# Performance work log

Hardware: AMD Instinct MI355X
Metric: run time of the kernel (lower is better)

## Reference

```python
import jax, jax.numpy as jnp
import numpy as np

# --- Mamba2Enc config (matches init_kwargs + mamba_ssm Mamba2 defaults) ---
D_IN = 1024
D_MODEL = 512
N_CLASSES = 2
NLAYERS = 2
D_STATE = 64
D_CONV = 4
EXPAND = 2
HEADDIM = 64
D_INNER = EXPAND * D_MODEL            # 1024
NHEADS = D_INNER // HEADDIM           # 16
CONV_DIM = D_INNER + 2 * D_STATE      # 1152 (ngroups=1)
D_IN_PROJ = 2 * D_INNER + 2 * D_STATE + NHEADS  # 2192
EPS = 1e-5


def setup_inputs() -> dict:
    key = jax.random.key(0)
    ks = jax.random.split(key, 10)
    def w(k, shape, sc=0.02):
        return jax.random.normal(k, shape, jnp.float32) * sc
    x = jax.random.normal(ks[0], (4, 4096, D_IN), jnp.float32)
    # fc1
    W1 = w(ks[1], (D_MODEL, D_IN))
    b1 = jnp.zeros((D_MODEL,), jnp.float32)
    # per-layer params stacked on leading NLAYERS axis
    ln_w = jnp.ones((NLAYERS, D_MODEL), jnp.float32)
    ln_b = jnp.zeros((NLAYERS, D_MODEL), jnp.float32)
    W_in = w(ks[2], (NLAYERS, D_IN_PROJ, D_MODEL))
    conv_w = w(ks[3], (NLAYERS, CONV_DIM, D_CONV), 0.1)
    conv_b = jnp.zeros((NLAYERS, CONV_DIM), jnp.float32)
    # dt_bias so that softplus(dt_bias) ~ [0.001, 0.1] (mamba init range)
    dt_bias = jax.random.uniform(ks[4], (NLAYERS, NHEADS), jnp.float32, -6.0, -2.3)
    A_log = jnp.log(jnp.tile(jnp.arange(1, NHEADS + 1, dtype=jnp.float32), (NLAYERS, 1)))
    Dskip = jnp.ones((NLAYERS, NHEADS), jnp.float32)
    norm_w = jnp.ones((NLAYERS, D_INNER), jnp.float32)
    W_out = w(ks[5], (NLAYERS, D_MODEL, D_INNER))
    # classifier
    Wc = w(ks[6], (N_CLASSES, D_MODEL))
    bc = jnp.zeros((N_CLASSES,), jnp.float32)
    return dict(x=x, W1=W1, b1=b1, ln_w=ln_w, ln_b=ln_b, W_in=W_in,
                conv_w=conv_w, conv_b=conv_b, dt_bias=dt_bias, A_log=A_log,
                Dskip=Dskip, norm_w=norm_w, W_out=W_out, Wc=Wc, bc=bc)


def _layernorm(h, w, b):
    mu = jnp.mean(h, axis=-1, keepdims=True)
    var = jnp.mean(jnp.square(h - mu), axis=-1, keepdims=True)
    return (h - mu) * jax.lax.rsqrt(var + EPS) * w + b


def _silu(x):
    return x * jax.nn.sigmoid(x)


def _mamba2(x, W_in, conv_w, conv_b, dt_bias, A_log, Dskip, norm_w, W_out):
    b, l, _ = x.shape
    zxbcdt = jnp.einsum('bld,ed->ble', x, W_in)  # (b, l, D_IN_PROJ)
    z = zxbcdt[..., :D_INNER]
    xBC = zxbcdt[..., D_INNER:D_INNER + CONV_DIM]
    dt = jax.nn.softplus(zxbcdt[..., -NHEADS:] + dt_bias)  # (b, l, h)
    # causal depthwise conv1d (kernel D_CONV) + silu
    xp = jnp.pad(xBC, ((0, 0), (D_CONV - 1, 0), (0, 0)))
    xBC = sum(xp[:, k:k + l, :] * conv_w[:, k] for k in range(D_CONV)) + conv_b
    xBC = _silu(xBC)
    xh = xBC[..., :D_INNER].reshape(b, l, NHEADS, HEADDIM)
    B = xBC[..., D_INNER:D_INNER + D_STATE]   # (b, l, n) ngroups=1
    C = xBC[..., D_INNER + D_STATE:]          # (b, l, n)
    A = -jnp.exp(A_log)                       # (h,)
    dA = jnp.exp(dt * A)                      # (b, l, h)
    dtx = dt[..., None] * xh                  # (b, l, h, p)

    def step(hstate, inp):
        dA_t, dtx_t, B_t, C_t = inp  # (b,h), (b,h,p), (b,n), (b,n)
        hstate = hstate * dA_t[:, :, None, None] + dtx_t[:, :, None, :] * B_t[:, None, :, None]
        y = jnp.einsum('bn,bhnp->bhp', C_t, hstate)
        return hstate, y

    init = jnp.zeros((b, NHEADS, D_STATE, HEADDIM), x.dtype)
    xs = (dA.transpose(1, 0, 2), dtx.transpose(1, 0, 2, 3),
          B.transpose(1, 0, 2), C.transpose(1, 0, 2))
    _, ys = jax.lax.scan(step, init, xs)      # ys: (l, b, h, p)
    y = ys.transpose(1, 0, 2, 3) + Dskip[None, None, :, None] * xh
    y = y.reshape(b, l, D_INNER)
    # RMSNormGated (norm_before_gate=False): rmsnorm(y * silu(z)) * weight
    y = y * _silu(z)
    y = y * jax.lax.rsqrt(jnp.mean(jnp.square(y), axis=-1, keepdims=True) + EPS) * norm_w
    return jnp.einsum('ble,de->bld', y, W_out)


def reference(x, W1, b1, ln_w, ln_b, W_in, conv_w, conv_b, dt_bias, A_log,
              Dskip, norm_w, W_out, Wc, bc):
    # fc1: Linear + GELU (dropout is identity at eval)
    h = jax.nn.gelu(jnp.einsum('bli,di->bld', x, W1) + b1, approximate=False)
    for i in range(NLAYERS):
        h = h + _mamba2(_layernorm(h, ln_w[i], ln_b[i]), W_in[i], conv_w[i],
                        conv_b[i], dt_bias[i], A_log[i], Dskip[i], norm_w[i], W_out[i])
    return jnp.einsum('bld,cd->blc', h, Wc) + bc
```

## Files before the change

kernel.cpp:

```cpp
#include <hip/hip_runtime.h>
#include <hip/hip_bf16.h>
#include <math.h>

#define BATCH 4
#define SEQ 4096
#define ROWS 16384
#define DIN 1024
#define DMODEL 512
#define DINNER 1024
#define DSTATE 64
#define NH 16
#define HD 64
#define CONVDIM 1152
#define DPROJ 2192
#define NPAD 2304
#define QC 64
#define NCH 64
#define LD 72

typedef __attribute__((ext_vector_type(8))) __bf16 bf16x8;
typedef __attribute__((ext_vector_type(4))) __bf16 bf16x4;
typedef __attribute__((ext_vector_type(4))) float f32x4;

__device__ __forceinline__ float siluf(float x){ return x / (1.f + __expf(-x)); }
__device__ __forceinline__ float geluf(float x){ return 0.5f*x*(1.f + erff(x*0.70710678118654752440f)); }

__device__ __forceinline__ bf16x8 scale8(bf16x8 v, float s){
  bf16x8 r;
  #pragma unroll
  for (int e = 0; e < 8; e++) r[e] = (__bf16)((float)v[e]*s);
  return r;
}

__device__ __forceinline__ void gl_lds16(const void* g, void* l){
  __builtin_amdgcn_global_load_lds((const __attribute__((address_space(1))) void*)g,
                                   (__attribute__((address_space(3))) void*)l, 16, 0, 0);
}

__global__ void cast_bf16_kernel(const float* __restrict__ src, __bf16* __restrict__ dst, long n){
  long i = (long)blockIdx.x*blockDim.x + threadIdx.x;
  long stride = (long)gridDim.x*blockDim.x;
  for (; i < n; i += stride) dst[i] = (__bf16)src[i];
}

__global__ void pad_win_kernel(const float* __restrict__ src, __bf16* __restrict__ dst){
  long total = 2L*NPAD*DMODEL;
  long i = (long)blockIdx.x*blockDim.x + threadIdx.x;
  long stride = (long)gridDim.x*blockDim.x;
  for (; i < total; i += stride){
    int k = (int)(i % DMODEL);
    int n = (int)((i / DMODEL) % NPAD);
    int l = (int)(i / ((long)DMODEL*NPAD));
    float v = (n < DPROJ) ? src[((long)l*DPROJ + n)*DMODEL + k] : 0.f;
    dst[i] = (__bf16)v;
  }
}

template<typename OutT, int EPI, int BM, int BN>
__global__ __launch_bounds__(256) void gemm_bt(const __bf16* __restrict__ A, const __bf16* __restrict__ Bm,
                                               OutT* __restrict__ C, const float* __restrict__ bias,
                                               int K, int Nc){
  constexpr int MI = BM/32, NI = BN/32;
  constexpr int CHA = BM/64;
  constexpr int CHT = (BM+BN)/64;
  __shared__ __align__(16) __bf16 As[BM*32];
  __shared__ __align__(16) __bf16 Bs[BN*32];
  int bm = blockIdx.x, bn = blockIdx.y;
  int tid = threadIdx.x;
  int lane = tid & 63, wid = tid >> 6;
  int wm = (wid >> 1)*(BM/2), wn = (wid & 1)*(BN/2);
  int lr = lane & 15, kb = lane >> 4;
  f32x4 acc[MI][NI] = {};
  const char* Ab = (const char*)A + (size_t)bm*BM*(size_t)(K*2);
  const char* Bb = (const char*)Bm + (size_t)bn*BN*(size_t)(K*2);
  int nkk = K >> 5;
  for (int kk = 0; kk < nkk; kk++){
    #pragma unroll
    for (int it = 0; it < CHT; it++){
      int cbase = it*4096 + wid*1024;
      int off = cbase + lane*16;
      int row = off >> 6, cb = off & 63;
      if (it < CHA) gl_lds16(Ab + (size_t)row*(K*2) + kk*64 + cb, (char*)As + cbase);
      else          gl_lds16(Bb + (size_t)(row - BM)*(K*2) + kk*64 + cb, (char*)Bs + (cbase - BM*64));
    }
    __syncthreads();
    bf16x8 af[MI], bfr[NI];
    #pragma unroll
    for (int mi = 0; mi < MI; mi++) af[mi] = *(const bf16x8*)(As + (wm + mi*16 + lr)*32 + kb*8);
    #pragma unroll
    for (int ni = 0; ni < NI; ni++) bfr[ni] = *(const bf16x8*)(Bs + (wn + ni*16 + lr)*32 + kb*8);
    #pragma unroll
    for (int mi = 0; mi < MI; mi++)
      #pragma unroll
      for (int ni = 0; ni < NI; ni++)
        acc[mi][ni] = __builtin_amdgcn_mfma_f32_16x16x32_bf16(af[mi], bfr[ni], acc[mi][ni], 0, 0, 0);
    __syncthreads();
  }
  #pragma unroll
  for (int mi = 0; mi < MI; mi++){
    #pragma unroll
    for (int ni = 0; ni < NI; ni++){
      int r0 = bm*BM + wm + mi*16 + (lane >> 4)*4;
      int c  = bn*BN + wn + ni*16 + lr;
      if (c < Nc){
        OutT* Cp = C + (size_t)r0*Nc + c;
        #pragma unroll
        for (int j = 0; j < 4; j++){
          float v = acc[mi][ni][j];
          if (EPI == 1){ float u = v + bias[c]; v = geluf(u); }
          if (EPI == 2){ v += (float)Cp[(size_t)j*Nc]; }
          Cp[(size_t)j*Nc] = (OutT)v;
        }
      }
    }
  }
}

__global__ __launch_bounds__(256) void ln_kernel(const float* __restrict__ h, const float* __restrict__ w,
                                                 const float* __restrict__ b, __bf16* __restrict__ out){
  int row = blockIdx.x*4 + (threadIdx.x >> 6);
  int lane = threadIdx.x & 63;
  const float* hr = h + (size_t)row*DMODEL + lane*8;
  float4 a = *(const float4*)hr, a2 = *(const float4*)(hr+4);
  float v[8] = {a.x,a.y,a.z,a.w,a2.x,a2.y,a2.z,a2.w};
  float s = 0.f;
  #pragma unroll
  for (int i = 0; i < 8; i++) s += v[i];
  #pragma unroll
  for (int o = 32; o; o >>= 1) s += __shfl_xor(s, o, 64);
  float mu = s*(1.f/512.f);
  float q = 0.f;
  #pragma unroll
  for (int i = 0; i < 8; i++){ float d = v[i]-mu; q += d*d; }
  #pragma unroll
  for (int o = 32; o; o >>= 1) q += __shfl_xor(q, o, 64);
  float rs = rsqrtf(q*(1.f/512.f) + 1e-5f);
  const float* wp = w + lane*8; const float* bp = b + lane*8;
  bf16x8 o8;
  #pragma unroll
  for (int i = 0; i < 8; i++) o8[i] = (__bf16)((v[i]-mu)*rs*wp[i] + bp[i]);
  *(bf16x8*)(out + (size_t)row*DMODEL + lane*8) = o8;
}

__global__ __launch_bounds__(256) void conv_bc(const __bf16* __restrict__ zx, const float* __restrict__ cw,
                                               const float* __restrict__ cb, __bf16* __restrict__ BCc){
  int idx = blockIdx.x*256 + threadIdx.x;
  int j = idx & 127;
  long bt = idx >> 7;
  int t = (int)(bt & (SEQ-1));
  int ch = DINNER + j;
  const __bf16* src = zx + (size_t)bt*DPROJ + 2048 + j;
  float acc = cb[ch] + (float)src[0]*cw[ch*4+3];
  if (t >= 1) acc += (float)src[-1L*DPROJ]*cw[ch*4+2];
  if (t >= 2) acc += (float)src[-2L*DPROJ]*cw[ch*4+1];
  if (t >= 3) acc += (float)src[-3L*DPROJ]*cw[ch*4+0];
  BCc[idx] = (__bf16)siluf(acc);
}

__global__ __launch_bounds__(256) void dt_kernel(const __bf16* __restrict__ zx, const float* __restrict__ dt_bias,
                                                 float* __restrict__ dtT){
  int idx = blockIdx.x*256 + threadIdx.x;
  int hh = idx & (NH-1); long bt = idx >> 4;
  int b = (int)(bt >> 12); int t = (int)(bt & (SEQ-1));
  float v = (float)zx[(size_t)bt*DPROJ + (DPROJ-NH) + hh] + dt_bias[hh];
  float sp = (v > 20.f) ? v : log1pf(__expf(v));
  dtT[((size_t)b*NH + hh)*SEQ + t] = sp;
}

__global__ __launch_bounds__(128) void ssd_state(const __bf16* __restrict__ zx, const __bf16* __restrict__ BCc,
                                                 const float* __restrict__ dtT, const float* __restrict__ A_log,
                                                 const float* __restrict__ cw, const float* __restrict__ cb,
                                                 __bf16* __restrict__ Schunk, float* __restrict__ Pbuf,
                                                 __bf16* __restrict__ xhT){
  __shared__ __align__(16) __bf16 Bt_all[2][64*LD];
  __shared__ __align__(16) __bf16 Xt_all[2][64*LD];
  int widx = threadIdx.x >> 6, lane = threadIdx.x & 63;
  int c = blockIdx.x*2 + widx, h = blockIdx.y, b = blockIdx.z;
  __bf16* Bt = Bt_all[widx];
  __bf16* Xt = Xt_all[widx];
  int lr = lane & 15, kb = lane >> 4, hi4 = lane >> 4;
  long t0 = (long)c*QC;
  size_t bt0 = (size_t)b*SEQ + t0;
  int bh = b*NH + h;
  float Ac = -expf(A_log[h]);
  float dtv = dtT[(size_t)bh*SEQ + t0 + lane];
  float cum = dtv*Ac;
  #pragma unroll
  for (int off = 1; off < 64; off <<= 1){ float v = __shfl_up(cum, off, 64); if (lane >= off) cum += v; }
  float cumQ = __shfl(cum, 63, 64);
  float w = __expf(cumQ - cum) * dtv;
  {
    const __bf16* bp = BCc + bt0*128 + lane;
    for (int tb = 0; tb < 8; tb++){
      bf16x8 buf;
      #pragma unroll
      for (int u = 0; u < 8; u++){
        int t = tb*8 + u;
        float bv = (float)bp[(size_t)t*128];
        buf[u] = (__bf16)(bv * __shfl(w, t, 64));
      }
      *(bf16x8*)&Bt[lane*LD + tb*8] = buf;
    }
  }
  {
    int ch = h*HD + lane;
    float w0 = cw[ch*4], w1 = cw[ch*4+1], w2 = cw[ch*4+2], w3 = cw[ch*4+3], cbv = cb[ch];
    const __bf16* xp = zx + bt0*DPROJ + (DINNER + ch);
    float x1 = (t0 >= 1) ? (float)xp[-1L*DPROJ] : 0.f;
    float x2 = (t0 >= 2) ? (float)xp[-2L*DPROJ] : 0.f;
    float x3 = (t0 >= 3) ? (float)xp[-3L*DPROJ] : 0.f;
    __bf16* xo = xhT + ((size_t)bh*NCH + c)*4096 + lane*64;
    for (int tb = 0; tb < 8; tb++){
      bf16x8 buf;
      #pragma unroll
      for (int u = 0; u < 8; u++){
        int t = tb*8 + u;
        float x0 = (float)xp[(size_t)t*DPROJ];
        float xv = siluf(cbv + w3*x0 + w2*x1 + w1*x2 + w0*x3);
        x3 = x2; x2 = x1; x1 = x0;
        buf[u] = (__bf16)xv;
      }
      *(bf16x8*)&Xt[lane*LD + tb*8] = buf;
      *(bf16x8*)(xo + tb*8) = buf;
    }
  }
  f32x4 acc[4][4] = {};
  #pragma unroll
  for (int kk = 0; kk < 2; kk++){
    bf16x8 af[4], bfr[4];
    #pragma unroll
    for (int mi = 0; mi < 4; mi++) af[mi]  = *(bf16x8*)&Bt[(mi*16+lr)*LD + kk*32 + kb*8];
    #pragma unroll
    for (int ni = 0; ni < 4; ni++) bfr[ni] = *(bf16x8*)&Xt[(ni*16+lr)*LD + kk*32 + kb*8];
    #pragma unroll
    for (int mi = 0; mi < 4; mi++)
      #pragma unroll
      for (int ni = 0; ni < 4; ni++)
        acc[mi][ni] = __builtin_amdgcn_mfma_f32_16x16x32_bf16(af[mi], bfr[ni], acc[mi][ni], 0, 0, 0);
  }
  __bf16* Sp = Schunk + ((size_t)bh*NCH + c)*4096;
  #pragma unroll
  for (int mi = 0; mi < 4; mi++)
    #pragma unroll
    for (int ni = 0; ni < 4; ni++){
      int n0 = mi*16 + hi4*4;
      int p  = ni*16 + lr;
      bf16x4 v;
      #pragma unroll
      for (int r = 0; r < 4; r++) v[r] = (__bf16)acc[mi][ni][r];
      *(bf16x4*)&Sp[p*64 + n0] = v;
    }
  if (lane == 0) Pbuf[bh*NCH + c] = __expf(cumQ);
}

__global__ __launch_bounds__(64) void ssd_comb(__bf16* __restrict__ Schunk, const float* __restrict__ Pbuf){
  int bh = blockIdx.x >> 4;
  int eb = blockIdx.x & 15;
  int e = eb*256 + threadIdx.x*4;
  __bf16* base = Schunk + (size_t)bh*NCH*4096 + e;
  float T0 = 0.f, T1 = 0.f, T2 = 0.f, T3 = 0.f;
  for (int c = 0; c < NCH; c++){
    float P = Pbuf[bh*NCH + c];
    bf16x4* p = (bf16x4*)(base + (size_t)c*4096);
    bf16x4 s = *p;
    bf16x4 o; o[0] = (__bf16)T0; o[1] = (__bf16)T1; o[2] = (__bf16)T2; o[3] = (__bf16)T3;
    *p = o;
    T0 = T0*P + (float)s[0]; T1 = T1*P + (float)s[1];
    T2 = T2*P + (float)s[2]; T3 = T3*P + (float)s[3];
  }
}

__global__ __launch_bounds__(256) void ssd_y(const __bf16* __restrict__ BCc, const float* __restrict__ dtT,
                                             const float* __restrict__ A_log, const float* __restrict__ Dskip,
                                             const __bf16* __restrict__ xhT, const __bf16* __restrict__ Spre,
                                             __bf16* __restrict__ yout){
  __shared__ __align__(16) __bf16 Gs_all[4][64*LD];
  __shared__ float cum_all[4][64], dt_all[4][64];
  int widx = threadIdx.x >> 6, lane = threadIdx.x & 63;
  int c = blockIdx.x*4 + widx, h = blockIdx.y, b = blockIdx.z;
  __bf16* Gs = Gs_all[widx];
  float* cum_s = cum_all[widx];
  float* dt_s = dt_all[widx];
  int lr = lane & 15, kb = lane >> 4, hi4 = lane >> 4;
  long t0 = (long)c*QC;
  size_t bt0 = (size_t)b*SEQ + t0;
  int bh = b*NH + h;
  float Ac = -expf(A_log[h]);
  float Dk = Dskip[h];
  float dtv = dtT[(size_t)bh*SEQ + t0 + lane];
  float cum = dtv*Ac;
  #pragma unroll
  for (int off = 1; off < 64; off <<= 1){ float v = __shfl_up(cum, off, 64); if (lane >= off) cum += v; }
  cum_s[lane] = cum; dt_s[lane] = dtv;
  bf16x8 cf[4][2];
  #pragma unroll
  for (int ni = 0; ni < 4; ni++)
    #pragma unroll
    for (int kk = 0; kk < 2; kk++)
      cf[ni][kk] = *(const bf16x8*)&BCc[(bt0 + ni*16 + lr)*128 + 64 + kk*32 + kb*8];
  f32x4 g[4][4] = {};
  #pragma unroll
  for (int kk = 0; kk < 2; kk++){
    bf16x8 bfj[4];
    #pragma unroll
    for (int mi = 0; mi < 4; mi++) bfj[mi] = *(const bf16x8*)&BCc[(bt0 + mi*16 + lr)*128 + kk*32 + kb*8];
    #pragma unroll
    for (int mi = 0; mi < 4; mi++)
      #pragma unroll
      for (int ni = 0; ni < 4; ni++)
        g[mi][ni] = __builtin_amdgcn_mfma_f32_16x16x32_bf16(bfj[mi], cf[ni][kk], g[mi][ni], 0, 0, 0);
  }
  float cumi[4];
  #pragma unroll
  for (int ni = 0; ni < 4; ni++) cumi[ni] = cum_s[ni*16 + lr];
  #pragma unroll
  for (int mi = 0; mi < 4; mi++){
    #pragma unroll
    for (int r = 0; r < 4; r++){
      int j = mi*16 + hi4*4 + r;
      float cj = cum_s[j], dj = dt_s[j];
      #pragma unroll
      for (int ni = 0; ni < 4; ni++){
        int i = ni*16 + lr;
        float v = g[mi][ni][r];
        if (i > j)       v = v * __expf(cumi[ni] - cj) * dj;
        else if (i == j) v = v*dj + Dk;
        else             v = 0.f;
        g[mi][ni][r] = v;
      }
    }
  }
  #pragma unroll
  for (int mi = 0; mi < 4; mi++)
    #pragma unroll
    for (int ni = 0; ni < 4; ni++){
      int j0 = mi*16 + hi4*4;
      int i  = ni*16 + lr;
      bf16x4 v;
      #pragma unroll
      for (int r = 0; r < 4; r++) v[r] = (__bf16)g[mi][ni][r];
      *(bf16x4*)&Gs[i*LD + j0] = v;
    }
  const __bf16* Xp = xhT + ((size_t)bh*NCH + c)*4096;
  f32x4 y4[4][4] = {};
  #pragma unroll
  for (int kk = 0; kk < 2; kk++){
    bf16x8 af2[4], bf2[4];
    #pragma unroll
    for (int mi = 0; mi < 4; mi++) af2[mi] = *(const bf16x8*)&Xp[(mi*16+lr)*64 + kk*32 + kb*8];
    #pragma unroll
    for (int ni = 0; ni < 4; ni++) bf2[ni] = *(bf16x8*)&Gs[(ni*16+lr)*LD + kk*32 + kb*8];
    #pragma unroll
    for (int mi = 0; mi < 4; mi++)
      #pragma unroll
      for (int ni = 0; ni < 4; ni++)
        y4[mi][ni] = __builtin_amdgcn_mfma_f32_16x16x32_bf16(af2[mi], bf2[ni], y4[mi][ni], 0, 0, 0);
  }
  {
    const __bf16* Sp = Spre + ((size_t)bh*NCH + c)*4096;
    float ei[4];
    #pragma unroll
    for (int ni = 0; ni < 4; ni++) ei[ni] = __expf(cumi[ni]);
    #pragma unroll
    for (int kk = 0; kk < 2; kk++){
      bf16x8 as1[4];
      #pragma unroll
      for (int mi = 0; mi < 4; mi++) as1[mi] = *(const bf16x8*)&Sp[(mi*16+lr)*64 + kk*32 + kb*8];
      #pragma unroll
      for (int ni = 0; ni < 4; ni++){
        bf16x8 cs = scale8(cf[ni][kk], ei[ni]);
        #pragma unroll
        for (int mi = 0; mi < 4; mi++)
          y4[mi][ni] = __builtin_amdgcn_mfma_f32_16x16x32_bf16(as1[mi], cs, y4[mi][ni], 0, 0, 0);
      }
    }
  }
  #pragma unroll
  for (int mi = 0; mi < 4; mi++)
    #pragma unroll
    for (int ni = 0; ni < 4; ni++){
      int p0 = mi*16 + hi4*4;
      int i  = ni*16 + lr;
      bf16x4 v;
      #pragma unroll
      for (int r = 0; r < 4; r++) v[r] = (__bf16)y4[mi][ni][r];
      *(bf16x4*)&yout[(bt0 + i)*DINNER + h*HD + p0] = v;
    }
}

__global__ __launch_bounds__(256) void gate_rms(__bf16* __restrict__ y, const __bf16* __restrict__ zx,
                                                const float* __restrict__ nw){
  int row = blockIdx.x*4 + (threadIdx.x >> 6);
  int lane = threadIdx.x & 63;
  __bf16* yr = y + (size_t)row*DINNER + lane*16;
  const __bf16* zr = zx + (size_t)row*DPROJ + lane*16;
  bf16x8 y0 = *(const bf16x8*)yr, y1 = *(const bf16x8*)(yr+8);
  bf16x8 z0 = *(const bf16x8*)zr, z1 = *(const bf16x8*)(zr+8);
  float v[16]; float ss = 0.f;
  #pragma unroll
  for (int i = 0; i < 8; i++){ float z = (float)z0[i]; float tv = (float)y0[i]*siluf(z); v[i] = tv; ss += tv*tv; }
  #pragma unroll
  for (int i = 0; i < 8; i++){ float z = (float)z1[i]; float tv = (float)y1[i]*siluf(z); v[8+i] = tv; ss += tv*tv; }
  #pragma unroll
  for (int o = 32; o; o >>= 1) ss += __shfl_xor(ss, o, 64);
  float rs = rsqrtf(ss*(1.f/1024.f) + 1e-5f);
  const float* np = nw + lane*16;
  bf16x8 o0, o1;
  #pragma unroll
  for (int i = 0; i < 8; i++){ o0[i] = (__bf16)(v[i]*rs*np[i]); o1[i] = (__bf16)(v[8+i]*rs*np[8+i]); }
  *(bf16x8*)yr = o0; *(bf16x8*)(yr+8) = o1;
}

__global__ __launch_bounds__(256) void cls_kernel(const float* __restrict__ h, const float* __restrict__ Wc,
                                                  const float* __restrict__ bc, float* __restrict__ out){
  int row = blockIdx.x*4 + (threadIdx.x >> 6);
  int lane = threadIdx.x & 63;
  const float* hr = h + (size_t)row*DMODEL + lane*8;
  float4 a = *(const float4*)hr, a2 = *(const float4*)(hr+4);
  float hv[8] = {a.x,a.y,a.z,a.w,a2.x,a2.y,a2.z,a2.w};
  const float* w0 = Wc + lane*8;
  const float* w1 = Wc + DMODEL + lane*8;
  float s0 = 0.f, s1 = 0.f;
  #pragma unroll
  for (int i = 0; i < 8; i++){ s0 += hv[i]*w0[i]; s1 += hv[i]*w1[i]; }
  #pragma unroll
  for (int o = 32; o; o >>= 1){ s0 += __shfl_xor(s0, o, 64); s1 += __shfl_xor(s1, o, 64); }
  if (lane == 0){ out[(size_t)row*2] = s0 + bc[0]; out[(size_t)row*2 + 1] = s1 + bc[1]; }
}

extern "C" void kernel_launch(void* const* d_in, const int* in_sizes, int n_in,
                              void* d_out, int out_size, void* d_ws, size_t ws_size,
                              hipStream_t stream){
  const float* x       = (const float*)d_in[0];
  const float* W1      = (const float*)d_in[1];
  const float* b1      = (const float*)d_in[2];
  const float* ln_w    = (const float*)d_in[3];
  const float* ln_b    = (const float*)d_in[4];
  const float* W_in    = (const float*)d_in[5];
  const float* conv_w  = (const float*)d_in[6];
  const float* conv_b  = (const float*)d_in[7];
  const float* dt_bias = (const float*)d_in[8];
  const float* A_log   = (const float*)d_in[9];
  const float* Dskip   = (const float*)d_in[10];
  const float* norm_w  = (const float*)d_in[11];
  const float* W_out   = (const float*)d_in[12];
  const float* Wc      = (const float*)d_in[13];
  const float* bc      = (const float*)d_in[14];
  float* out = (float*)d_out;
  char* ws = (char*)d_ws;

  size_t off = 0;
  auto alloc = [&](size_t bytes){ void* p = ws + off; off += (bytes + 255) & ~(size_t)255; return p; };
  char*   regionA = (char*) alloc((size_t)ROWS*DIN*2);
  __bf16* W1b     = (__bf16*)alloc((size_t)DMODEL*DIN*2);
  __bf16* Winb    = (__bf16*)alloc(2L*NPAD*DMODEL*2);
  __bf16* Woutb   = (__bf16*)alloc(2L*DMODEL*DINNER*2);
  float*  h       = (float*) alloc((size_t)ROWS*DMODEL*4);
  __bf16* zx      = (__bf16*)alloc((size_t)ROWS*DPROJ*2);
  __bf16* BCc     = (__bf16*)alloc((size_t)ROWS*128*2);
  float*  dtT     = (float*) alloc((size_t)ROWS*NH*4);
  __bf16* ybuf    = (__bf16*)alloc((size_t)ROWS*DINNER*2);
  __bf16* xhT     = (__bf16*)alloc((size_t)ROWS*DINNER*2);
  float*  Pbuf    = (float*) alloc(64L*NCH*4);
  if (off > ws_size) return;

  __bf16* x_bf   = (__bf16*)regionA;
  __bf16* hnb    = (__bf16*)regionA;
  __bf16* Schunk = (__bf16*)regionA;

  cast_bf16_kernel<<<4096, 256, 0, stream>>>(x, x_bf, (long)ROWS*DIN);
  cast_bf16_kernel<<<512, 256, 0, stream>>>(W1, W1b, (long)DMODEL*DIN);
  cast_bf16_kernel<<<1024, 256, 0, stream>>>(W_out, Woutb, 2L*DMODEL*DINNER);
  pad_win_kernel<<<2048, 256, 0, stream>>>(W_in, Winb);

  {
    dim3 g(ROWS/64, DMODEL/128);
    gemm_bt<float,1,64,128><<<g, 256, 0, stream>>>(x_bf, W1b, h, b1, DIN, DMODEL);
  }

  for (int l = 0; l < 2; l++){
    ln_kernel<<<ROWS/4, 256, 0, stream>>>(h, ln_w + l*DMODEL, ln_b + l*DMODEL, hnb);
    {
      dim3 g(ROWS/128, NPAD/128);
      gemm_bt<__bf16,0,128,128><<<g, 256, 0, stream>>>(hnb, Winb + (size_t)l*NPAD*DMODEL, zx, nullptr, DMODEL, DPROJ);
    }
    conv_bc<<<(ROWS*128)/256, 256, 0, stream>>>(zx, conv_w + l*CONVDIM*4, conv_b + l*CONVDIM, BCc);
    dt_kernel<<<(ROWS*NH)/256, 256, 0, stream>>>(zx, dt_bias + l*NH, dtT);
    {
      dim3 gs(NCH/2, NH, BATCH);
      ssd_state<<<gs, 128, 0, stream>>>(zx, BCc, dtT, A_log + l*NH,
                                        conv_w + l*CONVDIM*4, conv_b + l*CONVDIM, Schunk, Pbuf, xhT);
      ssd_comb<<<64*16, 64, 0, stream>>>(Schunk, Pbuf);
      dim3 gy(NCH/4, NH, BATCH);
      ssd_y<<<gy, 256, 0, stream>>>(BCc, dtT, A_log + l*NH, Dskip + l*NH, xhT, Schunk, ybuf);
    }
    gate_rms<<<ROWS/4, 256, 0, stream>>>(ybuf, zx, norm_w + l*DINNER);
    {
      dim3 g(ROWS/64, DMODEL/128);
      gemm_bt<float,2,64,128><<<g, 256, 0, stream>>>(ybuf, Woutb + (size_t)l*DMODEL*DINNER, h, nullptr, DINNER, DMODEL);
    }
  }

  cls_kernel<<<ROWS/4, 256, 0, stream>>>(h, Wc, bc, out);
}
```

Before: 510.6 us.

## Double-buffer LDS tiles in bf16 GEMM to overlap global loads with MFMA

Splits the GEMM shared-memory tiles into two buffers and issues the next k-slice's global-to-LDS loads before computing on the current slice. Partial vmcnt waits and raw s_barrier calls replace the full __syncthreads, so load latency can hide behind MFMA work. The cost is twice the LDS per block, which may lower occupancy. It also depends on the vmcnt count matching the number of loads issued per stage.

Measured after the change: 496.8 us. 2.7% less time.

```diff
diff --git a/kernel.cpp b/kernel.cpp
--- a/kernel.cpp
+++ b/kernel.cpp
@@ -63,8 +63,8 @@
   constexpr int MI = BM/32, NI = BN/32;
   constexpr int CHA = BM/64;
   constexpr int CHT = (BM+BN)/64;
-  __shared__ __align__(16) __bf16 As[BM*32];
-  __shared__ __align__(16) __bf16 Bs[BN*32];
+  __shared__ __align__(16) __bf16 As[2][BM*32];
+  __shared__ __align__(16) __bf16 Bs[2][BN*32];
   int bm = blockIdx.x, bn = blockIdx.y;
   int tid = threadIdx.x;
   int lane = tid & 63, wid = tid >> 6;
@@ -74,27 +74,44 @@
   const char* Ab = (const char*)A + (size_t)bm*BM*(size_t)(K*2);
   const char* Bb = (const char*)Bm + (size_t)bn*BN*(size_t)(K*2);
   int nkk = K >> 5;
-  for (int kk = 0; kk < nkk; kk++){
+
+  auto STAGE = [&](int kk, int buf){
     #pragma unroll
     for (int it = 0; it < CHT; it++){
       int cbase = it*4096 + wid*1024;
       int off = cbase + lane*16;
       int row = off >> 6, cb = off & 63;
-      if (it < CHA) gl_lds16(Ab + (size_t)row*(K*2) + kk*64 + cb, (char*)As + cbase);
-      else          gl_lds16(Bb + (size_t)(row - BM)*(K*2) + kk*64 + cb, (char*)Bs + (cbase - BM*64));
-    }
-    __syncthreads();
+      if (it < CHA) gl_lds16(Ab + (size_t)row*(K*2) + kk*64 + cb, (char*)(&As[buf][0]) + cbase);
+      else          gl_lds16(Bb + (size_t)(row - BM)*(K*2) + kk*64 + cb, (char*)(&Bs[buf][0]) + (cbase - BM*64));
+    }
+  };
+
+  STAGE(0, 0);
+  for (int kk = 0; kk < nkk; kk++){
+    int cur = kk & 1;
+    if (kk + 1 < nkk){
+      STAGE(kk + 1, cur ^ 1);
+      asm volatile("s_waitcnt vmcnt(%0)" :: "n"(CHT) : "memory");
+    } else {
+      asm volatile("s_waitcnt vmcnt(0)" ::: "memory");
+    }
+    __builtin_amdgcn_sched_barrier(0);
+    __builtin_amdgcn_s_barrier();
+    __builtin_amdgcn_sched_barrier(0);
+    const __bf16* Asb = &As[cur][0];
+    const __bf16* Bsb = &Bs[cur][0];
     bf16x8 af[MI], bfr[NI];
     #pragma unroll
-    for (int mi = 0; mi < MI; mi++) af[mi] = *(const bf16x8*)(As + (wm + mi*16 + lr)*32 + kb*8);
-    #pragma unroll
-    for (int ni = 0; ni < NI; ni++) bfr[ni] = *(const bf16x8*)(Bs + (wn + ni*16 + lr)*32 + kb*8);
+    for (int mi = 0; mi < MI; mi++) af[mi] = *(const bf16x8*)(Asb + (wm + mi*16 + lr)*32 + kb*8);
+    #pragma unroll
+    for (int ni = 0; ni < NI; ni++) bfr[ni] = *(const bf16x8*)(Bsb + (wn + ni*16 + lr)*32 + kb*8);
     #pragma unroll
     for (int mi = 0; mi < MI; mi++)
       #pragma unroll
       for (int ni = 0; ni < NI; ni++)
         acc[mi][ni] = __builtin_amdgcn_mfma_f32_16x16x32_bf16(af[mi], bfr[ni], acc[mi][ni], 0, 0, 0);
-    __syncthreads();
+    __builtin_amdgcn_s_barrier();
+    __builtin_amdgcn_sched_barrier(0);
   }
   #pragma unroll
   for (int mi = 0; mi < MI; mi++){
```
